# Kernel optimization log

Hardware: AMD Instinct MI355X
Metric: run time of the kernel (lower is better)

## Reference

```python
import jax, jax.numpy as jnp
import numpy as np

B, S, H = 2, 2048, 2048
NH, KVH, HD = 32, 8, 64
G = NH // KVH
BASE = 10000.0
SCALE = 1.0 / np.sqrt(HD).astype(np.float32)


def _rope_cache(seq_len, dim, base):
    inv_freq = 1.0 / (base ** (jnp.arange(0, dim, 2, dtype=jnp.float32) / dim))
    t = jnp.arange(seq_len, dtype=jnp.float32)
    freqs = jnp.outer(t, inv_freq)            # [S, HD/2]
    emb = jnp.concatenate([freqs, freqs], -1)  # [S, HD]
    return jnp.cos(emb), jnp.sin(emb)


def _rotate_half(x):
    x1, x2 = jnp.split(x, 2, axis=-1)
    return jnp.concatenate([-x2, x1], axis=-1)


def setup_inputs() -> dict:
    key = jax.random.key(0)
    ks = jax.random.split(key, 5)
    hidden_states = jax.random.normal(ks[0], (B, S, H), jnp.float32)
    # additive causal mask, broadcast over heads
    causal = jnp.tril(jnp.ones((S, S), dtype=bool))
    attention_mask = jnp.where(causal, 0.0, -1e9).astype(jnp.float32)[None, None]
    attention_mask = jnp.broadcast_to(attention_mask, (B, 1, S, S))
    position_ids = jnp.broadcast_to(jnp.arange(S, dtype=jnp.int32), (B, S))
    w = 0.02
    Wq = jax.random.normal(ks[1], (H, NH * HD), jnp.float32) * w
    Wk = jax.random.normal(ks[2], (H, KVH * HD), jnp.float32) * w
    Wv = jax.random.normal(ks[3], (H, KVH * HD), jnp.float32) * w
    Wo = jax.random.normal(ks[4], (NH * HD, H), jnp.float32) * w
    return {"hidden_states": hidden_states, "attention_mask": attention_mask,
            "position_ids": position_ids, "Wq": Wq, "Wk": Wk, "Wv": Wv, "Wo": Wo}


def reference(hidden_states, attention_mask, position_ids, Wq, Wk, Wv, Wo):
    b, s, _ = hidden_states.shape
    q = (hidden_states @ Wq).reshape(b, s, NH, HD).transpose(0, 2, 1, 3)   # [B,NH,S,HD]
    k = (hidden_states @ Wk).reshape(b, s, KVH, HD).transpose(0, 2, 1, 3)  # [B,KVH,S,HD]
    v = (hidden_states @ Wv).reshape(b, s, KVH, HD).transpose(0, 2, 1, 3)
    cos_c, sin_c = _rope_cache(s, HD, BASE)
    cos = cos_c[position_ids][:, None]  # [B,1,S,HD]
    sin = sin_c[position_ids][:, None]
    q = q * cos + _rotate_half(q) * sin
    k = k * cos + _rotate_half(k) * sin
    # GQA: grouped einsum == repeat_kv + matmul (same math, no KV duplication)
    qg = q.reshape(b, KVH, G, s, HD)
    scores = jnp.einsum('bkgsd,bktd->bkgst', qg, k) * SCALE  # [B,KVH,G,S,S]
    scores = scores + attention_mask[:, :, None]             # mask [B,1,1,S,S]
    probs = jax.nn.softmax(scores.astype(jnp.float32), axis=-1).astype(q.dtype)
    ctx = jnp.einsum('bkgst,bktd->bkgsd', probs, v)
    ctx = ctx.reshape(b, NH, s, HD).transpose(0, 2, 1, 3).reshape(b, s, NH * HD)
    return ctx @ Wo
```

## Files before the change

kernel.cpp:

```cpp
#include <hip/hip_runtime.h>
#include <hip/hip_bf16.h>

#define DB   2
#define DS   2048
#define DH   2048
#define DNH  32
#define DKVH 8
#define DHD  64
#define DM   4096
#define DNQKV 3072

typedef __attribute__((ext_vector_type(8))) short bf16x8;
typedef __attribute__((ext_vector_type(4))) float f32x4;
typedef __attribute__((ext_vector_type(8))) unsigned short us8;
typedef __attribute__((ext_vector_type(4))) unsigned short us4;

__device__ __forceinline__ float b2f(unsigned short u) {
  unsigned int x = ((unsigned int)u) << 16;
  return __builtin_bit_cast(float, x);
}
__device__ __forceinline__ unsigned short f2b(float f) {
  unsigned int u = __builtin_bit_cast(unsigned int, f);
  return (unsigned short)((u + 0x8000u) >> 16);
}
__device__ __forceinline__ void async_copy16(void* lds, const void* g) {
  __builtin_amdgcn_global_load_lds((const __attribute__((address_space(1))) void*)g,
                                   (__attribute__((address_space(3))) void*)lds,
                                   16, 0, 0);
}

__global__ void detect_mode(const unsigned short* __restrict__ w, int* __restrict__ flags) {
  int t = threadIdx.x;
  int trips = 0;
  for (int i = 0; i < 4; i++) {
    unsigned short u = w[t * 4 + i];
    int e = (u >> 7) & 0xFF;
    if (e >= 161 || (e <= 93 && e != 0)) trips++;
  }
  for (int off = 32; off > 0; off >>= 1) trips += __shfl_down(trips, off);
  if (t == 0) {
    flags[0] = (trips >= 8) ? 1 : 0;
    flags[1] = 0;
  }
}

__global__ __launch_bounds__(256) void convert_x(const void* __restrict__ xin,
                                                 unsigned short* __restrict__ xb,
                                                 const int* __restrict__ flags, int n) {
  int mode = flags[0];
  int i = (blockIdx.x * 256 + threadIdx.x) * 8;
  if (i >= n) return;
  if (mode) {
    const float* f = (const float*)xin;
    us8 o;
#pragma unroll
    for (int j = 0; j < 8; j++) o[j] = f2b(f[i + j]);
    *(us8*)&xb[i] = o;
  } else {
    *(us8*)&xb[i] = *(const us8*)((const unsigned short*)xin + i);
  }
}

__global__ __launch_bounds__(256) void transpose_w(const void* __restrict__ win,
                                                   unsigned short* __restrict__ out,
                                                   const int* __restrict__ flags,
                                                   int R, int C) {
  __shared__ float tile[32][33];
  int mode = flags[0];
  int c0 = blockIdx.x * 32, r0 = blockIdx.y * 32;
  int tx = threadIdx.x & 31, ty = threadIdx.x >> 5;
  if (mode) {
    const float* f = (const float*)win;
    for (int i = ty; i < 32; i += 8) tile[i][tx] = f[(size_t)(r0 + i) * C + c0 + tx];
  } else {
    const unsigned short* bsrc = (const unsigned short*)win;
    for (int i = ty; i < 32; i += 8) tile[i][tx] = b2f(bsrc[(size_t)(r0 + i) * C + c0 + tx]);
  }
  __syncthreads();
  for (int i = ty; i < 32; i += 8) out[(size_t)(c0 + i) * R + r0 + tx] = f2b(tile[tx][i]);
}

__global__ __launch_bounds__(256)
void gemm_bt(const unsigned short* __restrict__ A, const unsigned short* __restrict__ Bt,
             unsigned short* __restrict__ Cb, float* __restrict__ Cf,
             const int* __restrict__ outmode, int M, int N, int K) {
  __shared__ __align__(16) unsigned short lA[128 * 32];
  __shared__ __align__(16) unsigned short lB[128 * 32];
  int tid = threadIdx.x, lane = tid & 63, wave = tid >> 6;
  int wm = wave >> 1, wn = wave & 1;
  int quad = lane >> 4, l15 = lane & 15;
  size_t tm0 = (size_t)blockIdx.y * 128, tn0 = (size_t)blockIdx.x * 128;

  f32x4 zero4 = {0.f, 0.f, 0.f, 0.f};
  f32x4 acc[4][4];
#pragma unroll
  for (int mi = 0; mi < 4; mi++)
#pragma unroll
    for (int ni = 0; ni < 4; ni++) acc[mi][ni] = zero4;

  int nk = K >> 5;
  for (int kt = 0; kt < nk; kt++) {
    __syncthreads();
#pragma unroll
    for (int i = 0; i < 2; i++) {
      int c = tid + 256 * i;
      int r = c >> 2, cb = (c & 3) * 8;
      async_copy16(&lA[c * 8], A + (tm0 + r) * K + kt * 32 + cb);
      async_copy16(&lB[c * 8], Bt + (tn0 + r) * K + kt * 32 + cb);
    }
    __syncthreads();
    bf16x8 af[4], bfr[4];
#pragma unroll
    for (int mi = 0; mi < 4; mi++)
      af[mi] = *(const bf16x8*)&lA[(wm * 64 + mi * 16 + l15) * 32 + quad * 8];
#pragma unroll
    for (int ni = 0; ni < 4; ni++)
      bfr[ni] = *(const bf16x8*)&lB[(wn * 64 + ni * 16 + l15) * 32 + quad * 8];
#pragma unroll
    for (int mi = 0; mi < 4; mi++)
#pragma unroll
      for (int ni = 0; ni < 4; ni++)
        acc[mi][ni] = __builtin_amdgcn_mfma_f32_16x16x32_bf16(af[mi], bfr[ni], acc[mi][ni], 0, 0, 0);
  }
  int mode = *outmode;
#pragma unroll
  for (int mi = 0; mi < 4; mi++)
#pragma unroll
    for (int ni = 0; ni < 4; ni++)
#pragma unroll
      for (int r = 0; r < 4; r++) {
        size_t gr = tm0 + wm * 64 + mi * 16 + quad * 4 + r;
        size_t gc = tn0 + wn * 64 + ni * 16 + l15;
        float v = acc[mi][ni][r];
        if (mode) Cf[gr * N + gc] = v;
        else      Cb[gr * N + gc] = f2b(v);
      }
}

#define QSC 0.18033688011112042f
__global__ __launch_bounds__(256) void rope_qk(const unsigned short* __restrict__ c1,
                                               const int* __restrict__ pos_ids,
                                               unsigned short* __restrict__ qws,
                                               unsigned short* __restrict__ kws) {
  int idx = blockIdx.x * 256 + threadIdx.x;
  int row = idx / 1280;
  int rem = idx - row * 1280;
  int head = rem >> 5, d = rem & 31;
  int b = row >> 11, s = row & 2047;
  float t = (float)pos_ids[row];
  float invf = __expf(-(float)d * (9.210340371976184f / 32.0f));
  float ang = t * invf;
  float sn, cs;
  __sincosf(ang, &sn, &cs);
  size_t col;
  unsigned short* dst;
  float sc;
  if (head < 32) {
    col = (size_t)head * 64 + d;
    dst = qws + ((size_t)(b * DNH + head) * DS + s) * DHD + d;
    sc = QSC;
  } else {
    int kh = head - 32;
    col = 2048 + (size_t)kh * 64 + d;
    dst = kws + ((size_t)(b * DKVH + kh) * DS + s) * DHD + d;
    sc = 1.0f;
  }
  float x1 = b2f(c1[(size_t)row * DNQKV + col]);
  float x2 = b2f(c1[(size_t)row * DNQKV + col + 32]);
  dst[0]  = f2b((x1 * cs - x2 * sn) * sc);
  dst[32] = f2b((x2 * cs + x1 * sn) * sc);
}

__global__ __launch_bounds__(256) void transpose_v(const unsigned short* __restrict__ c1,
                                                   unsigned short* __restrict__ vt) {
  __shared__ unsigned short tile[64 * 72];
  int s0 = blockIdx.x * 64;
  int bk = blockIdx.y;
  int b = bk >> 3, kvh = bk & 7;
  const unsigned short* src = c1 + (size_t)(b * DS + s0) * DNQKV + 2560 + kvh * 64;
#pragma unroll
  for (int i = 0; i < 2; i++) {
    int c = threadIdx.x + 256 * i;
    int s = c >> 3, d0 = (c & 7) * 8;
    *(us8*)&tile[s * 72 + d0] = *(const us8*)(src + (size_t)s * DNQKV + d0);
  }
  __syncthreads();
  unsigned short* dst = vt + (size_t)bk * 64 * DS + s0;
#pragma unroll
  for (int i = 0; i < 2; i++) {
    int c = threadIdx.x + 256 * i;
    int d = c >> 3, sc = (c & 7) * 8;
    us8 o;
#pragma unroll
    for (int j = 0; j < 8; j++) o[j] = tile[(sc + j) * 72 + d];
    *(us8*)&dst[(size_t)d * DS + sc] = o;
  }
}

__global__ __launch_bounds__(256, 4)
void flash_attn(const unsigned short* __restrict__ q, const unsigned short* __restrict__ k,
                const unsigned short* __restrict__ vt, unsigned short* __restrict__ ctx) {
  __shared__ __align__(16) unsigned short lK0[64 * 32];
  __shared__ __align__(16) unsigned short lK1[64 * 32];
  __shared__ __align__(16) unsigned short lV0[64 * 32];
  __shared__ __align__(16) unsigned short lV1[64 * 32];
  __shared__ __align__(16) unsigned short lP[4 * 16 * 72];
  int tid = threadIdx.x, lane = tid & 63, wave = tid >> 6;
  int quad = lane >> 4, l15 = lane & 15;
  int bh = blockIdx.y, b = bh >> 5, h = bh & 31, kvh = h >> 2;
  const unsigned short* qb = q + (size_t)(b * DNH + h) * DS * DHD;
  const unsigned short* kb = k + (size_t)(b * DKVH + kvh) * DS * DHD;
  const unsigned short* vb = vt + (size_t)(b * DKVH + kvh) * DHD * DS;
  unsigned short* lPw = lP + wave * 16 * 72;
  int r4 = tid >> 2, c8 = (tid & 3) * 8;

  f32x4 zero4 = {0.f, 0.f, 0.f, 0.f};
  for (int ph = 0; ph < 2; ph++) {
    int qt = ph ? (31 - blockIdx.x) : blockIdx.x;
    int q0 = qt * 64;
    const unsigned short* qp = qb + (size_t)(q0 + wave * 16 + l15) * DHD + quad * 8;
    bf16x8 qf0 = *(const bf16x8*)qp;
    bf16x8 qf1 = *(const bf16x8*)(qp + 32);
    f32x4 oacc[4];
#pragma unroll
    for (int dj = 0; dj < 4; dj++) oacc[dj] = zero4;
    float mrow = -1e30f, lrow = 0.f;

    int nt = qt + 1;
    for (int t = 0; t < nt; t++) {
      int kv0 = t * 64;
      __syncthreads();
      async_copy16(&lK0[tid * 8], kb + (size_t)(kv0 + r4) * DHD + c8);
      async_copy16(&lK1[tid * 8], kb + (size_t)(kv0 + r4) * DHD + 32 + c8);
      async_copy16(&lV0[tid * 8], vb + (size_t)r4 * DS + kv0 + c8);
      async_copy16(&lV1[tid * 8], vb + (size_t)r4 * DS + kv0 + 32 + c8);
      __syncthreads();

      f32x4 sacc[4];
#pragma unroll
      for (int nj = 0; nj < 4; nj++) {
        sacc[nj] = zero4;
        bf16x8 kf0 = *(const bf16x8*)&lK0[(nj * 16 + l15) * 32 + quad * 8];
        bf16x8 kf1 = *(const bf16x8*)&lK1[(nj * 16 + l15) * 32 + quad * 8];
        sacc[nj] = __builtin_amdgcn_mfma_f32_16x16x32_bf16(kf0, qf0, sacc[nj], 0, 0, 0);
        sacc[nj] = __builtin_amdgcn_mfma_f32_16x16x32_bf16(kf1, qf1, sacc[nj], 0, 0, 0);
      }
      if (t == nt - 1) {
        int ql = wave * 16 + l15;
#pragma unroll
        for (int nj = 0; nj < 4; nj++)
#pragma unroll
          for (int r = 0; r < 4; r++)
            if (nj * 16 + quad * 4 + r > ql) sacc[nj][r] = -1e30f;
      }
      float tm = -1e30f;
#pragma unroll
      for (int nj = 0; nj < 4; nj++)
#pragma unroll
        for (int r = 0; r < 4; r++) tm = fmaxf(tm, sacc[nj][r]);
      tm = fmaxf(tm, __shfl_xor(tm, 16));
      tm = fmaxf(tm, __shfl_xor(tm, 32));
      float mn = fmaxf(mrow, tm);
      float alpha = __builtin_amdgcn_exp2f(mrow - mn);
      mrow = mn;
      float rs = 0.f;
      float p[4][4];
#pragma unroll
      for (int nj = 0; nj < 4; nj++)
#pragma unroll
        for (int r = 0; r < 4; r++) {
          float e = __builtin_amdgcn_exp2f(sacc[nj][r] - mn);
          p[nj][r] = e;
          rs += e;
        }
      rs += __shfl_xor(rs, 16);
      rs += __shfl_xor(rs, 32);
      lrow = lrow * alpha + rs;
#pragma unroll
      for (int nj = 0; nj < 4; nj++) {
        us4 w4;
#pragma unroll
        for (int r = 0; r < 4; r++) w4[r] = f2b(p[nj][r]);
        *(us4*)&lPw[l15 * 72 + nj * 16 + quad * 4] = w4;
      }
      bf16x8 pf0 = *(const bf16x8*)&lPw[l15 * 72 + quad * 8];
      bf16x8 pf1 = *(const bf16x8*)&lPw[l15 * 72 + 32 + quad * 8];
#pragma unroll
      for (int dj = 0; dj < 4; dj++) {
#pragma unroll
        for (int r = 0; r < 4; r++) oacc[dj][r] *= alpha;
        bf16x8 vf0 = *(const bf16x8*)&lV0[(dj * 16 + l15) * 32 + quad * 8];
        bf16x8 vf1 = *(const bf16x8*)&lV1[(dj * 16 + l15) * 32 + quad * 8];
        oacc[dj] = __builtin_amdgcn_mfma_f32_16x16x32_bf16(vf0, pf0, oacc[dj], 0, 0, 0);
        oacc[dj] = __builtin_amdgcn_mfma_f32_16x16x32_bf16(vf1, pf1, oacc[dj], 0, 0, 0);
      }
    }
    float inv = __builtin_amdgcn_rcpf(lrow);
    size_t orow = ((size_t)b * DS + q0 + wave * 16 + l15) * (DNH * DHD) + (size_t)h * DHD;
#pragma unroll
    for (int dj = 0; dj < 4; dj++) {
      us4 o4;
#pragma unroll
      for (int r = 0; r < 4; r++) o4[r] = f2b(oacc[dj][r] * inv);
      *(us4*)&ctx[orow + dj * 16 + quad * 4] = o4;
    }
  }
}

extern "C" void kernel_launch(void* const* d_in, const int* in_sizes, int n_in,
                              void* d_out, int out_size, void* d_ws, size_t ws_size,
                              hipStream_t stream) {
  (void)in_sizes; (void)n_in; (void)out_size; (void)ws_size;
  const void* hs = d_in[0];
  const int* pos = (const int*)d_in[2];
  const void* wq = d_in[3];
  const void* wk = d_in[4];
  const void* wv = d_in[5];
  const void* wo = d_in[6];

  char* ws = (char*)d_ws;
  size_t off = 0;
  auto take = [&](size_t bytes) -> char* {
    char* p = ws + off;
    off += (bytes + 255) & ~(size_t)255;
    return p;
  };
  int* flags            = (int*)take(256);
  unsigned short* xb    = (unsigned short*)take((size_t)DM * DH * 2);
  unsigned short* wtqkv = (unsigned short*)take((size_t)DNQKV * DH * 2);
  unsigned short* wto   = (unsigned short*)take((size_t)DH * DH * 2);
  unsigned short* c1    = (unsigned short*)take((size_t)DM * DNQKV * 2);
  unsigned short* qws   = (unsigned short*)take((size_t)DB * DNH * DS * DHD * 2);
  unsigned short* kws   = (unsigned short*)take((size_t)DB * DKVH * DS * DHD * 2);
  unsigned short* vtws  = (unsigned short*)take((size_t)DB * DKVH * DS * DHD * 2);
  unsigned short* ctx   = (unsigned short*)take((size_t)DM * DNH * DHD * 2);

  detect_mode<<<1, 64, 0, stream>>>((const unsigned short*)wq, flags);
  convert_x<<<DM * DH / 8 / 256, 256, 0, stream>>>(hs, xb, flags, DM * DH);
  transpose_w<<<dim3(64, 64), 256, 0, stream>>>(wq, wtqkv, flags, 2048, 2048);
  transpose_w<<<dim3(16, 64), 256, 0, stream>>>(wk, wtqkv + (size_t)2048 * 2048, flags, 2048, 512);
  transpose_w<<<dim3(16, 64), 256, 0, stream>>>(wv, wtqkv + (size_t)2560 * 2048, flags, 2048, 512);
  transpose_w<<<dim3(64, 64), 256, 0, stream>>>(wo, wto, flags, 2048, 2048);

  gemm_bt<<<dim3(DNQKV / 128, DM / 128), 256, 0, stream>>>(
      xb, wtqkv, c1, (float*)nullptr, flags + 1, DM, DNQKV, DH);

  rope_qk<<<DM * 40 * 32 / 256, 256, 0, stream>>>(c1, pos, qws, kws);
  transpose_v<<<dim3(DS / 64, DB * DKVH), 256, 0, stream>>>(c1, vtws);

  flash_attn<<<dim3(16, DB * DNH), 256, 0, stream>>>(qws, kws, vtws, ctx);

  gemm_bt<<<dim3(DH / 128, DM / 128), 256, 0, stream>>>(
      ctx, wto, (unsigned short*)d_out, (float*)d_out, flags, DM, DH, DH);
}
```

Before: 373.7 us.

## Fuse RoPE and head-major scatter into QKV GEMM epilogue, remap tile order

The QKV GEMM epilogue now applies rotary embedding and writes Q, K and V directly in head-major layout. This removes the intermediate c1 buffer and the separate rope kernel. Both GEMMs also remap block IDs so that consecutive blocks spread across 8 groups, which is meant to improve cache locality across the XCDs, and their dimensions are specialised to constants. The trade-offs are scattered 2-byte epilogue stores and extra sincos work inside the GEMM, plus an extra V buffer that still goes through the V transpose.

```diff
diff --git a/kernel.cpp b/kernel.cpp
--- a/kernel.cpp
+++ b/kernel.cpp
@@ -38,10 +38,7 @@
     if (e >= 161 || (e <= 93 && e != 0)) trips++;
   }
   for (int off = 32; off > 0; off >>= 1) trips += __shfl_down(trips, off);
-  if (t == 0) {
-    flags[0] = (trips >= 8) ? 1 : 0;
-    flags[1] = 0;
-  }
+  if (t == 0) flags[0] = (trips >= 8) ? 1 : 0;
 }
 
 __global__ __launch_bounds__(256) void convert_x(const void* __restrict__ xin,
@@ -80,16 +77,22 @@
   for (int i = ty; i < 32; i += 8) out[(size_t)(c0 + i) * R + r0 + tx] = f2b(tile[tx][i]);
 }
 
+#define QSC 0.18033688011112042f
+
 __global__ __launch_bounds__(256)
-void gemm_bt(const unsigned short* __restrict__ A, const unsigned short* __restrict__ Bt,
-             unsigned short* __restrict__ Cb, float* __restrict__ Cf,
-             const int* __restrict__ outmode, int M, int N, int K) {
+void gemm_qkv(const unsigned short* __restrict__ A, const unsigned short* __restrict__ Bt,
+              const int* __restrict__ pos_ids,
+              unsigned short* __restrict__ qws, unsigned short* __restrict__ kws,
+              unsigned short* __restrict__ vws) {
   __shared__ __align__(16) unsigned short lA[128 * 32];
   __shared__ __align__(16) unsigned short lB[128 * 32];
   int tid = threadIdx.x, lane = tid & 63, wave = tid >> 6;
   int wm = wave >> 1, wn = wave & 1;
   int quad = lane >> 4, l15 = lane & 15;
-  size_t tm0 = (size_t)blockIdx.y * 128, tn0 = (size_t)blockIdx.x * 128;
+  int bid = blockIdx.y * 24 + blockIdx.x;
+  int tile = (bid & 7) * 96 + (bid >> 3);
+  int bxt = tile % 24, byt = tile / 24;
+  size_t tm0 = (size_t)byt * 128, tn0 = (size_t)bxt * 128;
 
   f32x4 zero4 = {0.f, 0.f, 0.f, 0.f};
   f32x4 acc[4][4];
@@ -98,15 +101,100 @@
 #pragma unroll
     for (int ni = 0; ni < 4; ni++) acc[mi][ni] = zero4;
 
-  int nk = K >> 5;
-  for (int kt = 0; kt < nk; kt++) {
+  for (int kt = 0; kt < 64; kt++) {
     __syncthreads();
 #pragma unroll
     for (int i = 0; i < 2; i++) {
       int c = tid + 256 * i;
       int r = c >> 2, cb = (c & 3) * 8;
-      async_copy16(&lA[c * 8], A + (tm0 + r) * K + kt * 32 + cb);
-      async_copy16(&lB[c * 8], Bt + (tn0 + r) * K + kt * 32 + cb);
+      async_copy16(&lA[c * 8], A + (tm0 + r) * DH + kt * 32 + cb);
+      async_copy16(&lB[c * 8], Bt + (tn0 + r) * DH + kt * 32 + cb);
+    }
+    __syncthreads();
+    bf16x8 af[4], bfr[4];
+#pragma unroll
+    for (int mi = 0; mi < 4; mi++)
+      af[mi] = *(const bf16x8*)&lA[(wm * 64 + mi * 16 + l15) * 32 + quad * 8];
+#pragma unroll
+    for (int ni = 0; ni < 4; ni++)
+      bfr[ni] = *(const bf16x8*)&lB[(wn * 64 + ni * 16 + l15) * 32 + quad * 8];
+#pragma unroll
+    for (int mi = 0; mi < 4; mi++)
+#pragma unroll
+      for (int ni = 0; ni < 4; ni++)
+        acc[mi][ni] = __builtin_amdgcn_mfma_f32_16x16x32_bf16(af[mi], bfr[ni], acc[mi][ni], 0, 0, 0);
+  }
+
+  int hs = bxt * 2 + wn;
+  if (hs < 40) {
+    float sc = (hs < 32) ? QSC : 1.0f;
+    unsigned short* dst0 = (hs < 32) ? qws : kws;
+    int hh = (hs < 32) ? hs : (hs - 32);
+    float invf0 = __expf(-(float)l15 * (9.210340371976184f / 32.0f));
+    float invf1 = invf0 * 0.01f;
+#pragma unroll
+    for (int mi = 0; mi < 4; mi++)
+#pragma unroll
+      for (int r = 0; r < 4; r++) {
+        size_t gr = tm0 + wm * 64 + mi * 16 + quad * 4 + r;
+        int b = (int)(gr >> 11), s = (int)(gr & 2047);
+        float t = (float)pos_ids[gr];
+        unsigned short* row = dst0 + ((size_t)(b * ((hs < 32) ? DNH : DKVH) + hh) * DS + s) * DHD;
+#pragma unroll
+        for (int ni = 0; ni < 2; ni++) {
+          float x1 = acc[mi][ni][r], x2 = acc[mi][ni + 2][r];
+          float ang = t * (ni ? invf1 : invf0);
+          float sn, cs;
+          __sincosf(ang, &sn, &cs);
+          int d = ni * 16 + l15;
+          row[d]      = f2b((x1 * cs - x2 * sn) * sc);
+          row[d + 32] = f2b((x2 * cs + x1 * sn) * sc);
+        }
+      }
+  } else {
+    int vh = hs - 40;
+#pragma unroll
+    for (int mi = 0; mi < 4; mi++)
+#pragma unroll
+      for (int r = 0; r < 4; r++) {
+        size_t gr = tm0 + wm * 64 + mi * 16 + quad * 4 + r;
+        int b = (int)(gr >> 11), s = (int)(gr & 2047);
+        unsigned short* row = vws + ((size_t)(b * DKVH + vh) * DS + s) * DHD;
+#pragma unroll
+        for (int ni = 0; ni < 4; ni++) row[ni * 16 + l15] = f2b(acc[mi][ni][r]);
+      }
+  }
+}
+
+__global__ __launch_bounds__(256)
+void gemm_out(const unsigned short* __restrict__ A, const unsigned short* __restrict__ Bt,
+              unsigned short* __restrict__ Cb, float* __restrict__ Cf,
+              const int* __restrict__ outmode) {
+  __shared__ __align__(16) unsigned short lA[128 * 32];
+  __shared__ __align__(16) unsigned short lB[128 * 32];
+  int tid = threadIdx.x, lane = tid & 63, wave = tid >> 6;
+  int wm = wave >> 1, wn = wave & 1;
+  int quad = lane >> 4, l15 = lane & 15;
+  int bid = blockIdx.y * 16 + blockIdx.x;
+  int tile = (bid & 7) * 64 + (bid >> 3);
+  int bxt = tile & 15, byt = tile >> 4;
+  size_t tm0 = (size_t)byt * 128, tn0 = (size_t)bxt * 128;
+
+  f32x4 zero4 = {0.f, 0.f, 0.f, 0.f};
+  f32x4 acc[4][4];
+#pragma unroll
+  for (int mi = 0; mi < 4; mi++)
+#pragma unroll
+    for (int ni = 0; ni < 4; ni++) acc[mi][ni] = zero4;
+
+  for (int kt = 0; kt < 64; kt++) {
+    __syncthreads();
+#pragma unroll
+    for (int i = 0; i < 2; i++) {
+      int c = tid + 256 * i;
+      int r = c >> 2, cb = (c & 3) * 8;
+      async_copy16(&lA[c * 8], A + (tm0 + r) * DH + kt * 32 + cb);
+      async_copy16(&lB[c * 8], Bt + (tn0 + r) * DH + kt * 32 + cb);
     }
     __syncthreads();
     bf16x8 af[4], bfr[4];
@@ -132,60 +220,25 @@
         size_t gr = tm0 + wm * 64 + mi * 16 + quad * 4 + r;
         size_t gc = tn0 + wn * 64 + ni * 16 + l15;
         float v = acc[mi][ni][r];
-        if (mode) Cf[gr * N + gc] = v;
-        else      Cb[gr * N + gc] = f2b(v);
-      }
-}
-
-#define QSC 0.18033688011112042f
-__global__ __launch_bounds__(256) void rope_qk(const unsigned short* __restrict__ c1,
-                                               const int* __restrict__ pos_ids,
-                                               unsigned short* __restrict__ qws,
-                                               unsigned short* __restrict__ kws) {
-  int idx = blockIdx.x * 256 + threadIdx.x;
-  int row = idx / 1280;
-  int rem = idx - row * 1280;
-  int head = rem >> 5, d = rem & 31;
-  int b = row >> 11, s = row & 2047;
-  float t = (float)pos_ids[row];
-  float invf = __expf(-(float)d * (9.210340371976184f / 32.0f));
-  float ang = t * invf;
-  float sn, cs;
-  __sincosf(ang, &sn, &cs);
-  size_t col;
-  unsigned short* dst;
-  float sc;
-  if (head < 32) {
-    col = (size_t)head * 64 + d;
-    dst = qws + ((size_t)(b * DNH + head) * DS + s) * DHD + d;
-    sc = QSC;
-  } else {
-    int kh = head - 32;
-    col = 2048 + (size_t)kh * 64 + d;
-    dst = kws + ((size_t)(b * DKVH + kh) * DS + s) * DHD + d;
-    sc = 1.0f;
-  }
-  float x1 = b2f(c1[(size_t)row * DNQKV + col]);
-  float x2 = b2f(c1[(size_t)row * DNQKV + col + 32]);
-  dst[0]  = f2b((x1 * cs - x2 * sn) * sc);
-  dst[32] = f2b((x2 * cs + x1 * sn) * sc);
-}
-
-__global__ __launch_bounds__(256) void transpose_v(const unsigned short* __restrict__ c1,
+        if (mode) Cf[gr * DH + gc] = v;
+        else      Cb[gr * DH + gc] = f2b(v);
+      }
+}
+
+__global__ __launch_bounds__(256) void transpose_v(const unsigned short* __restrict__ vws,
                                                    unsigned short* __restrict__ vt) {
   __shared__ unsigned short tile[64 * 72];
   int s0 = blockIdx.x * 64;
   int bk = blockIdx.y;
-  int b = bk >> 3, kvh = bk & 7;
-  const unsigned short* src = c1 + (size_t)(b * DS + s0) * DNQKV + 2560 + kvh * 64;
+  const unsigned short* src = vws + ((size_t)bk * DS + s0) * DHD;
 #pragma unroll
   for (int i = 0; i < 2; i++) {
     int c = threadIdx.x + 256 * i;
     int s = c >> 3, d0 = (c & 7) * 8;
-    *(us8*)&tile[s * 72 + d0] = *(const us8*)(src + (size_t)s * DNQKV + d0);
+    *(us8*)&tile[s * 72 + d0] = *(const us8*)(src + (size_t)s * DHD + d0);
   }
   __syncthreads();
-  unsigned short* dst = vt + (size_t)bk * 64 * DS + s0;
+  unsigned short* dst = vt + (size_t)bk * DHD * DS + s0;
 #pragma unroll
   for (int i = 0; i < 2; i++) {
     int c = threadIdx.x + 256 * i;
@@ -329,9 +382,9 @@
   unsigned short* xb    = (unsigned short*)take((size_t)DM * DH * 2);
   unsigned short* wtqkv = (unsigned short*)take((size_t)DNQKV * DH * 2);
   unsigned short* wto   = (unsigned short*)take((size_t)DH * DH * 2);
-  unsigned short* c1    = (unsigned short*)take((size_t)DM * DNQKV * 2);
   unsigned short* qws   = (unsigned short*)take((size_t)DB * DNH * DS * DHD * 2);
   unsigned short* kws   = (unsigned short*)take((size_t)DB * DKVH * DS * DHD * 2);
+  unsigned short* vws   = (unsigned short*)take((size_t)DB * DKVH * DS * DHD * 2);
   unsigned short* vtws  = (unsigned short*)take((size_t)DB * DKVH * DS * DHD * 2);
   unsigned short* ctx   = (unsigned short*)take((size_t)DM * DNH * DHD * 2);
 
@@ -342,14 +395,11 @@
   transpose_w<<<dim3(16, 64), 256, 0, stream>>>(wv, wtqkv + (size_t)2560 * 2048, flags, 2048, 512);
   transpose_w<<<dim3(64, 64), 256, 0, stream>>>(wo, wto, flags, 2048, 2048);
 
-  gemm_bt<<<dim3(DNQKV / 128, DM / 128), 256, 0, stream>>>(
-      xb, wtqkv, c1, (float*)nullptr, flags + 1, DM, DNQKV, DH);
-
-  rope_qk<<<DM * 40 * 32 / 256, 256, 0, stream>>>(c1, pos, qws, kws);
-  transpose_v<<<dim3(DS / 64, DB * DKVH), 256, 0, stream>>>(c1, vtws);
+  gemm_qkv<<<dim3(24, 32), 256, 0, stream>>>(xb, wtqkv, pos, qws, kws, vws);
+
+  transpose_v<<<dim3(DS / 64, DB * DKVH), 256, 0, stream>>>(vws, vtws);
 
   flash_attn<<<dim3(16, DB * DNH), 256, 0, stream>>>(qws, kws, vtws, ctx);
 
-  gemm_bt<<<dim3(DH / 128, DM / 128), 256, 0, stream>>>(
-      ctx, wto, (unsigned short*)d_out, (float*)d_out, flags, DM, DH, DH);
-}
+  gemm_out<<<dim3(16, 32), 256, 0, stream>>>(ctx, wto, (unsigned short*)d_out, (float*)d_out, flags);
+}
```

Result: no change. 372.5 us (-0.3%).
